# Kernel tuning notes

Hardware: AMD Instinct MI355X
Metric: run time of the kernel (lower is better)

The kernel has to match this reference:

```python
import jax, jax.numpy as jnp
import numpy as np

HID = 64   # hidden_dim
T = 256    # number of time points
B = 2048   # batch of initial conditions
DT = 0.05  # time step (t grid spacing)


def _xavier(k, shape, gain=0.5):
    fan_out, fan_in = shape
    std = gain * np.sqrt(2.0 / (fan_in + fan_out))
    return jax.random.normal(k, shape, dtype=jnp.float32) * std


def setup_inputs() -> dict:
    key = jax.random.key(0)
    ks = jax.random.split(key, 4)
    return {
        "t": jnp.arange(T, dtype=jnp.float32) * DT,
        "x0": jax.random.normal(ks[0], (B, 2), dtype=jnp.float32),
        "W1": _xavier(ks[1], (HID, 2)),
        "b1": jnp.zeros((HID,), jnp.float32),
        "W2": _xavier(ks[2], (HID, HID)),
        "b2": jnp.zeros((HID,), jnp.float32),
        "W3": _xavier(ks[3], (1, HID)),
        "b3": jnp.zeros((1,), jnp.float32),
    }


def reference(t, x0, W1, b1, W2, b2, W3, b3):
    """RK4 rollout of Hamiltonian dynamics. Returns trajectory [T, B, 2]."""

    def dynamics(x):
        h1 = jnp.tanh(x @ W1.T + b1)          # [B, H]
        h2 = jnp.tanh(h1 @ W2.T + b2)         # [B, H]
        # Analytic dH/dx via reverse chain (equivalent to autograd.grad):
        g2 = (1.0 - h2 * h2) * W3[0]          # [B, H]
        g1 = (1.0 - h1 * h1) * (g2 @ W2)      # [B, H]
        dHdx = g1 @ W1                        # [B, 2]  -> (dH/dq, dH/dp)
        # Hamilton's equations: dq/dt = dH/dp, dp/dt = -dH/dq
        return jnp.stack([dHdx[..., 1], -dHdx[..., 0]], axis=-1)

    dt = t[1] - t[0]

    def step(x, _):
        k1 = dynamics(x)
        k2 = dynamics(x + 0.5 * dt * k1)
        k3 = dynamics(x + 0.5 * dt * k2)
        k4 = dynamics(x + dt * k3)
        x_new = x + (dt / 6.0) * (k1 + 2.0 * k2 + 2.0 * k3 + k4)
        return x_new, x_new

    _, ys = jax.lax.scan(step, x0, None, length=t.shape[0] - 1)
    return jnp.concatenate([x0[None], ys], axis=0)  # [T, B, 2]
```

## Files before the change

kernel.cpp:

```cpp
#include <hip/hip_runtime.h>

#define HID    64
#define TSTEPS 256
#define BATCH  2048

typedef float v2f __attribute__((ext_vector_type(2)));

__device__ __forceinline__ float fast_tanh(float x) {
    float e = __builtin_amdgcn_exp2f(x * 2.8853900817779268f);
    float r = __builtin_amdgcn_rcpf(e + 1.0f);
    return fmaf(-2.0f, r, 1.0f);
}

template <int M>
__device__ __forceinline__ float swz(float v) {
    return __int_as_float(__builtin_amdgcn_ds_swizzle(
        __float_as_int(v), (M << 10) | 0x1F));
}
template <int M>
__device__ __forceinline__ v2f swz2(v2f v) {
    v2f r; r.x = swz<M>(v.x); r.y = swz<M>(v.y); return r;
}

template <int CTRL>
__device__ __forceinline__ float dppf(float x) {
    int xi = __float_as_int(x);
    return __int_as_float(__builtin_amdgcn_update_dpp(xi, xi, CTRL, 0xF, 0xF, false));
}
template <int CTRL>
__device__ __forceinline__ v2f dpp2(v2f v) {
    v2f r; r.x = dppf<CTRL>(v.x); r.y = dppf<CTRL>(v.y); return r;
}

__device__ __forceinline__ float bperm(int addr, float v) {
    return __int_as_float(__builtin_amdgcn_ds_bpermute(addr, __float_as_int(v)));
}

__global__ __launch_bounds__(256, 2) void hnn_rk4_kernel(
        const float* __restrict__ tarr,
        const float* __restrict__ x0,
        const float* __restrict__ W1,
        const float* __restrict__ b1,
        const float* __restrict__ W2,
        const float* __restrict__ b2,
        const float* __restrict__ W3,
        float* __restrict__ out)
{
    const int lane = threadIdx.x & 63;
    const int wid  = threadIdx.x >> 6;
    const int b    = blockIdx.x * 4 + wid;

    const int r0 = (lane >> 3) << 3;
    const int c0 = (lane & 7) << 3;

    const float dt  = tarr[1] - tarr[0];
    const float hdt = 0.5f * dt;
    const float sdt = dt * (1.0f / 6.0f);

    v2f   w1v = *(const v2f*)(W1 + 2 * lane);
    float b1i = b1[lane];
    float b2i = b2[lane];
    float w3i = W3[lane];

    int ba[8];
#pragma unroll
    for (int t = 0; t < 8; ++t) ba[t] = (c0 + t) * 4;
    int a32 = (lane ^ 32) * 4;

    v2f wfT[32], wbT[32];
#pragma unroll
    for (int t = 0; t < 8; ++t) {
#pragma unroll
        for (int m = 0; m < 4; ++m) {
            v2f f;
            f.x = W2[(r0 + 2 * m)     * HID + c0 + t];
            f.y = W2[(r0 + 2 * m + 1) * HID + c0 + t];
            wfT[t * 4 + m] = f;
            wbT[t * 4 + m] = *(const v2f*)(W2 + (c0 + t) * HID + r0 + 2 * m);
        }
    }

#pragma unroll
    for (int k = 0; k < 32; ++k) {
        asm volatile("" : "+v"(wfT[k]), "+v"(wbT[k]));
    }
#pragma unroll
    for (int t = 0; t < 8; ++t) asm volatile("" : "+v"(ba[t]));
    asm volatile("" : "+v"(w1v), "+v"(b1i), "+v"(b2i), "+v"(w3i), "+v"(a32));

    const bool s1b = lane & 1, s2b = lane & 2, s4b = lane & 4;

    auto reduce_pairs = [&](v2f P0, v2f P1, v2f P2, v2f P3) -> float {
        v2f kA0 = s2b ? P1 : P0,  sA0 = s2b ? P0 : P1;
        v2f kA1 = s2b ? P3 : P2,  sA1 = s2b ? P2 : P3;
        v2f g0 = kA0 + dpp2<0x4E>(sA0);
        v2f g1 = kA1 + dpp2<0x4E>(sA1);
        v2f kB = s4b ? g1 : g0,   sB = s4b ? g0 : g1;
        v2f h  = kB + swz2<4>(sB);
        v2f vf = h + dpp2<0xB1>(h);
        return s1b ? vf.y : vf.x;
    };

    float q = x0[2 * b + 0];
    float p = x0[2 * b + 1];

    if (lane == 0) {
        out[2 * b + 0] = q;
        out[2 * b + 1] = p;
    }

    auto dynamics = [&](float xq, float xp, float& kq, float& kp) {
        const float h1 = fast_tanh(fmaf(w1v.x, xq, fmaf(w1v.y, xp, b1i)));

        float hb[8];
#pragma unroll
        for (int t = 0; t < 8; ++t) hb[t] = bperm(ba[t], h1);

        v2f P0 = {0.f, 0.f}, P1 = {0.f, 0.f}, P2 = {0.f, 0.f}, P3 = {0.f, 0.f};
#pragma unroll
        for (int t = 0; t < 8; ++t) {
            v2f hh; hh.x = hb[t]; hh.y = hb[t];
            P0 = __builtin_elementwise_fma(wfT[t * 4 + 0], hh, P0);
            P1 = __builtin_elementwise_fma(wfT[t * 4 + 1], hh, P1);
            P2 = __builtin_elementwise_fma(wfT[t * 4 + 2], hh, P2);
            P3 = __builtin_elementwise_fma(wfT[t * 4 + 3], hh, P3);
        }
        const float pre2 = reduce_pairs(P0, P1, P2, P3) + b2i;
        const float h2   = fast_tanh(pre2);
        const float g2   = w3i * fmaf(-h2, h2, 1.0f);

        float gb[8];
#pragma unroll
        for (int t = 0; t < 8; ++t) gb[t] = bperm(ba[t], g2);

        v2f Q0 = {0.f, 0.f}, Q1 = {0.f, 0.f}, Q2 = {0.f, 0.f}, Q3 = {0.f, 0.f};
#pragma unroll
        for (int t = 0; t < 8; ++t) {
            v2f gg; gg.x = gb[t]; gg.y = gb[t];
            Q0 = __builtin_elementwise_fma(wbT[t * 4 + 0], gg, Q0);
            Q1 = __builtin_elementwise_fma(wbT[t * 4 + 1], gg, Q1);
            Q2 = __builtin_elementwise_fma(wbT[t * 4 + 2], gg, Q2);
            Q3 = __builtin_elementwise_fma(wbT[t * 4 + 3], gg, Q3);
        }
        const float u  = reduce_pairs(Q0, Q1, Q2, Q3);
        const float g1 = u * fmaf(-h1, h1, 1.0f);

        v2f gv; gv.x = g1; gv.y = g1;
        v2f sv = w1v * gv;
        sv = sv + dpp2<0xB1>(sv);
        sv = sv + dpp2<0x4E>(sv);
        sv = sv + swz2<4>(sv);
        sv = sv + swz2<8>(sv);
        sv = sv + swz2<16>(sv);
        v2f sw; sw.x = bperm(a32, sv.x); sw.y = bperm(a32, sv.y);
        sv = sv + sw;
        kq = sv.y;
        kp = -sv.x;
    };

#pragma unroll 1
    for (int s = 0; s < TSTEPS - 1; ++s) {
        float kq1, kp1, kq2, kp2, kq3, kp3, kq4, kp4;
        dynamics(q, p, kq1, kp1);
        dynamics(fmaf(hdt, kq1, q), fmaf(hdt, kp1, p), kq2, kp2);
        dynamics(fmaf(hdt, kq2, q), fmaf(hdt, kp2, p), kq3, kp3);
        dynamics(fmaf(dt,  kq3, q), fmaf(dt,  kp3, p), kq4, kp4);
        q = fmaf(sdt, kq1 + 2.f * kq2 + 2.f * kq3 + kq4, q);
        p = fmaf(sdt, kp1 + 2.f * kp2 + 2.f * kp3 + kp4, p);
        if (lane == 0) {
            out[(s + 1) * (BATCH * 2) + 2 * b + 0] = q;
            out[(s + 1) * (BATCH * 2) + 2 * b + 1] = p;
        }
    }
}

extern "C" void kernel_launch(void* const* d_in, const int* in_sizes, int n_in,
                              void* d_out, int out_size, void* d_ws, size_t ws_size,
                              hipStream_t stream) {
    const float* t  = (const float*)d_in[0];
    const float* x0 = (const float*)d_in[1];
    const float* W1 = (const float*)d_in[2];
    const float* b1 = (const float*)d_in[3];
    const float* W2 = (const float*)d_in[4];
    const float* b2 = (const float*)d_in[5];
    const float* W3 = (const float*)d_in[6];

    hnn_rk4_kernel<<<dim3(BATCH / 4), dim3(256), 0, stream>>>(
        t, x0, W1, b1, W2, b2, W3, (float*)d_out);
}
```

Baseline: 830.1 us.

## Reuse forward W2 tile for backward matvec, dropping the transposed W2 copy

The backward product g2 @ W2 now reuses the same per-lane W2 tile as the forward pass. Each lane broadcasts g2 along the row index instead of the column index, and the partial sums are reduced across row groups with DPP, swizzle and bpermute, followed by a bit-reversed permute to restore lane order. This removes the 32 extra v2f registers that held the transposed W2 copy, freeing registers and possibly allowing higher occupancy. In exchange the backward reduction uses more cross-lane operations, and one swizzle in the final reduction becomes a DPP row operation.

Result: slower. 869.4 us (+4.7%).

```diff
diff --git a/kernel.cpp b/kernel.cpp
--- a/kernel.cpp
+++ b/kernel.cpp
@@ -50,8 +50,8 @@
     const int wid  = threadIdx.x >> 6;
     const int b    = blockIdx.x * 4 + wid;
 
-    const int r0 = (lane >> 3) << 3;
-    const int c0 = (lane & 7) << 3;
+    const int rr = lane >> 3,  cc = lane & 7;
+    const int r0 = rr << 3,    c0 = cc << 3;
 
     const float dt  = tarr[1] - tarr[0];
     const float hdt = 0.5f * dt;
@@ -62,12 +62,17 @@
     float b2i = b2[lane];
     float w3i = W3[lane];
 
-    int ba[8];
-#pragma unroll
-    for (int t = 0; t < 8; ++t) ba[t] = (c0 + t) * 4;
+    int ba[8], br[8];
+#pragma unroll
+    for (int t = 0; t < 8; ++t) {
+        ba[t] = (c0 + t) * 4;
+        br[t] = (r0 + t) * 4;
+    }
     int a32 = (lane ^ 32) * 4;
-
-    v2f wfT[32], wbT[32];
+    const int rv = ((cc & 1) << 2) | (cc & 2) | ((cc >> 2) & 1);
+    int atr = (8 * rv + rr) * 4;
+
+    v2f wfT[32];
 #pragma unroll
     for (int t = 0; t < 8; ++t) {
 #pragma unroll
@@ -76,19 +81,11 @@
             f.x = W2[(r0 + 2 * m)     * HID + c0 + t];
             f.y = W2[(r0 + 2 * m + 1) * HID + c0 + t];
             wfT[t * 4 + m] = f;
-            wbT[t * 4 + m] = *(const v2f*)(W2 + (c0 + t) * HID + r0 + 2 * m);
-        }
-    }
-
-#pragma unroll
-    for (int k = 0; k < 32; ++k) {
-        asm volatile("" : "+v"(wfT[k]), "+v"(wbT[k]));
-    }
-#pragma unroll
-    for (int t = 0; t < 8; ++t) asm volatile("" : "+v"(ba[t]));
-    asm volatile("" : "+v"(w1v), "+v"(b1i), "+v"(b2i), "+v"(w3i), "+v"(a32));
-
-    const bool s1b = lane & 1, s2b = lane & 2, s4b = lane & 4;
+        }
+    }
+
+    const bool s1b = lane & 1,  s2b = lane & 2,  s4b = lane & 4;
+    const bool rb0 = lane & 8,  rb1 = lane & 16, rb2 = lane & 32;
 
     auto reduce_pairs = [&](v2f P0, v2f P1, v2f P2, v2f P3) -> float {
         v2f kA0 = s2b ? P1 : P0,  sA0 = s2b ? P0 : P1;
@@ -127,22 +124,43 @@
         }
         const float pre2 = reduce_pairs(P0, P1, P2, P3) + b2i;
         const float h2   = fast_tanh(pre2);
-        const float g2   = w3i * fmaf(-h2, h2, 1.0f);
+        const float g2v  = w3i * fmaf(-h2, h2, 1.0f);
 
         float gb[8];
 #pragma unroll
-        for (int t = 0; t < 8; ++t) gb[t] = bperm(ba[t], g2);
-
-        v2f Q0 = {0.f, 0.f}, Q1 = {0.f, 0.f}, Q2 = {0.f, 0.f}, Q3 = {0.f, 0.f};
+        for (int t = 0; t < 8; ++t) gb[t] = bperm(br[t], g2v);
+        v2f gp[4];
+#pragma unroll
+        for (int m = 0; m < 4; ++m) { gp[m].x = gb[2 * m]; gp[m].y = gb[2 * m + 1]; }
+
+        float uP[8];
 #pragma unroll
         for (int t = 0; t < 8; ++t) {
-            v2f gg; gg.x = gb[t]; gg.y = gb[t];
-            Q0 = __builtin_elementwise_fma(wbT[t * 4 + 0], gg, Q0);
-            Q1 = __builtin_elementwise_fma(wbT[t * 4 + 1], gg, Q1);
-            Q2 = __builtin_elementwise_fma(wbT[t * 4 + 2], gg, Q2);
-            Q3 = __builtin_elementwise_fma(wbT[t * 4 + 3], gg, Q3);
-        }
-        const float u  = reduce_pairs(Q0, Q1, Q2, Q3);
+            v2f acc = gp[0] * wfT[t * 4 + 0];
+            acc = __builtin_elementwise_fma(gp[1], wfT[t * 4 + 1], acc);
+            acc = __builtin_elementwise_fma(gp[2], wfT[t * 4 + 2], acc);
+            acc = __builtin_elementwise_fma(gp[3], wfT[t * 4 + 3], acc);
+            uP[t] = acc.x + acc.y;
+        }
+
+        float v4[4];
+#pragma unroll
+        for (int t = 0; t < 4; ++t) {
+            float keep = rb0 ? uP[t + 4] : uP[t];
+            float send = rb0 ? uP[t]     : uP[t + 4];
+            v4[t] = keep + dppf<0x128>(send);
+        }
+        float w2v[2];
+#pragma unroll
+        for (int k = 0; k < 2; ++k) {
+            float keep = rb1 ? v4[k + 2] : v4[k];
+            float send = rb1 ? v4[k]     : v4[k + 2];
+            w2v[k] = keep + swz<16>(send);
+        }
+        float keep3 = rb2 ? w2v[1] : w2v[0];
+        float send3 = rb2 ? w2v[0] : w2v[1];
+        float upre  = keep3 + bperm(a32, send3);
+        const float u  = bperm(atr, upre);
         const float g1 = u * fmaf(-h1, h1, 1.0f);
 
         v2f gv; gv.x = g1; gv.y = g1;
@@ -150,7 +168,7 @@
         sv = sv + dpp2<0xB1>(sv);
         sv = sv + dpp2<0x4E>(sv);
         sv = sv + swz2<4>(sv);
-        sv = sv + swz2<8>(sv);
+        sv = sv + dpp2<0x128>(sv);
         sv = sv + swz2<16>(sv);
         v2f sw; sw.x = bperm(a32, sv.x); sw.y = bperm(a32, sv.y);
         sv = sv + sw;
@@ -160,6 +178,12 @@
 
 #pragma unroll 1
     for (int s = 0; s < TSTEPS - 1; ++s) {
+#pragma unroll
+        for (int k = 0; k < 32; ++k) asm volatile("" : "+v"(wfT[k]));
+#pragma unroll
+        for (int t = 0; t < 8; ++t) asm volatile("" : "+v"(ba[t]), "+v"(br[t]));
+        asm volatile("" : "+v"(a32), "+v"(atr));
+
         float kq1, kp1, kq2, kp2, kq3, kp3, kq4, kp4;
         dynamics(q, p, kq1, kp1);
         dynamics(fmaf(hdt, kq1, q), fmaf(hdt, kp1, p), kq2, kp2);
```

## Permute hidden-unit layout to shorten cross-lane reductions and use DPP row-broadcast sums

Applied to the files above, without the earlier changes.

Reassigns hidden units to lanes with a bit-reversed permutation and stores W2 slices pre-XORed, so the partial-sum reductions after each 64x64 matvec need fewer, cheaper DPP/swizzle steps without lane-dependent selects. The final gradient reduction becomes a DPP row_shr/row_bcast scan followed by readlane, and inline v_pk_fma_f32 asm forces packed FMAs. It also drops the register-pinning asm barriers and changes launch bounds to 1 wave-group per CU minimum. This adds an extra bpermute to transpose the backward result and relies on the hand-written reduction being correct.

Measured after the change: 790.2 us. 1.05x faster.

```diff
diff --git a/kernel.cpp b/kernel.cpp
--- a/kernel.cpp
+++ b/kernel.cpp
@@ -17,26 +17,38 @@
     return __int_as_float(__builtin_amdgcn_ds_swizzle(
         __float_as_int(v), (M << 10) | 0x1F));
 }
-template <int M>
-__device__ __forceinline__ v2f swz2(v2f v) {
-    v2f r; r.x = swz<M>(v.x); r.y = swz<M>(v.y); return r;
-}
 
 template <int CTRL>
-__device__ __forceinline__ float dppf(float x) {
+__device__ __forceinline__ float dppx(float x) {
     int xi = __float_as_int(x);
     return __int_as_float(__builtin_amdgcn_update_dpp(xi, xi, CTRL, 0xF, 0xF, false));
-}
-template <int CTRL>
-__device__ __forceinline__ v2f dpp2(v2f v) {
-    v2f r; r.x = dppf<CTRL>(v.x); r.y = dppf<CTRL>(v.y); return r;
 }
 
 __device__ __forceinline__ float bperm(int addr, float v) {
     return __int_as_float(__builtin_amdgcn_ds_bpermute(addr, __float_as_int(v)));
 }
 
-__global__ __launch_bounds__(256, 2) void hnn_rk4_kernel(
+__device__ __forceinline__ void pkfma(v2f& acc, v2f w, v2f hv) {
+    asm("v_pk_fma_f32 %0, %1, %2, %0" : "+v"(acc) : "v"(w), "v"(hv));
+}
+
+__device__ __forceinline__ float wave_sum(float v) {
+    v += dppx<0x121>(v);
+    v += dppx<0x122>(v);
+    v += dppx<0x124>(v);
+    v += dppx<0x128>(v);
+    v += __int_as_float(__builtin_amdgcn_update_dpp(
+            0, __float_as_int(v), 0x142, 0xA, 0xF, false));
+    v += __int_as_float(__builtin_amdgcn_update_dpp(
+            0, __float_as_int(v), 0x143, 0xC, 0xF, false));
+    return __int_as_float(__builtin_amdgcn_readlane(__float_as_int(v), 63));
+}
+
+__device__ __forceinline__ int rev3(int x) {
+    return ((x & 1) << 2) | (x & 2) | ((x >> 2) & 1);
+}
+
+__global__ __launch_bounds__(256, 1) void hnn_rk4_kernel(
         const float* __restrict__ tarr,
         const float* __restrict__ x0,
         const float* __restrict__ W1,
@@ -50,56 +62,44 @@
     const int wid  = threadIdx.x >> 6;
     const int b    = blockIdx.x * 4 + wid;
 
-    const int r0 = (lane >> 3) << 3;
-    const int c0 = (lane & 7) << 3;
+    const int rr = lane >> 3, cc = lane & 7;
+    const int pc = rev3(cc),  pr = rev3(rr);
+    const int uo = 8 * rr + pc;
 
     const float dt  = tarr[1] - tarr[0];
     const float hdt = 0.5f * dt;
     const float sdt = dt * (1.0f / 6.0f);
 
-    v2f   w1v = *(const v2f*)(W1 + 2 * lane);
-    float b1i = b1[lane];
-    float b2i = b2[lane];
-    float w3i = W3[lane];
+    const float w1a = W1[2 * uo + 0];
+    const float w1b = W1[2 * uo + 1];
+    const float b1i = b1[uo];
+    const float b2i = b2[uo];
+    const float w3i = W3[uo];
 
-    int ba[8];
+    int ba[8], br[8];
 #pragma unroll
-    for (int t = 0; t < 8; ++t) ba[t] = (c0 + t) * 4;
+    for (int t = 0; t < 8; ++t) {
+        ba[t] = (8 * cc + rev3(t)) * 4;
+        br[t] = (8 * rr + rev3(t)) * 4;
+    }
     int a32 = (lane ^ 32) * 4;
+    int atr = (8 * cc + rr) * 4;
 
-    v2f wfT[32], wbT[32];
+    v2f wsF[8][4], wsB[8][4];
 #pragma unroll
     for (int t = 0; t < 8; ++t) {
 #pragma unroll
         for (int m = 0; m < 4; ++m) {
             v2f f;
-            f.x = W2[(r0 + 2 * m)     * HID + c0 + t];
-            f.y = W2[(r0 + 2 * m + 1) * HID + c0 + t];
-            wfT[t * 4 + m] = f;
-            wbT[t * 4 + m] = *(const v2f*)(W2 + (c0 + t) * HID + r0 + 2 * m);
+            f.x = W2[(8 * rr + ((2 * m)     ^ pc)) * HID + 8 * cc + t];
+            f.y = W2[(8 * rr + ((2 * m + 1) ^ pc)) * HID + 8 * cc + t];
+            wsF[t][m] = f;
+            v2f g;
+            g.x = W2[(8 * rr + t) * HID + 8 * cc + ((2 * m)     ^ pr)];
+            g.y = W2[(8 * rr + t) * HID + 8 * cc + ((2 * m + 1) ^ pr)];
+            wsB[t][m] = g;
         }
     }
-
-#pragma unroll
-    for (int k = 0; k < 32; ++k) {
-        asm volatile("" : "+v"(wfT[k]), "+v"(wbT[k]));
-    }
-#pragma unroll
-    for (int t = 0; t < 8; ++t) asm volatile("" : "+v"(ba[t]));
-    asm volatile("" : "+v"(w1v), "+v"(b1i), "+v"(b2i), "+v"(w3i), "+v"(a32));
-
-    const bool s1b = lane & 1, s2b = lane & 2, s4b = lane & 4;
-
-    auto reduce_pairs = [&](v2f P0, v2f P1, v2f P2, v2f P3) -> float {
-        v2f kA0 = s2b ? P1 : P0,  sA0 = s2b ? P0 : P1;
-        v2f kA1 = s2b ? P3 : P2,  sA1 = s2b ? P2 : P3;
-        v2f g0 = kA0 + dpp2<0x4E>(sA0);
-        v2f g1 = kA1 + dpp2<0x4E>(sA1);
-        v2f kB = s4b ? g1 : g0,   sB = s4b ? g0 : g1;
-        v2f h  = kB + swz2<4>(sB);
-        v2f vf = h + dpp2<0xB1>(h);
-        return s1b ? vf.y : vf.x;
-    };
 
     float q = x0[2 * b + 0];
     float p = x0[2 * b + 1];
@@ -110,7 +110,7 @@
     }
 
     auto dynamics = [&](float xq, float xp, float& kq, float& kp) {
-        const float h1 = fast_tanh(fmaf(w1v.x, xq, fmaf(w1v.y, xp, b1i)));
+        const float h1 = fast_tanh(fmaf(w1a, xq, fmaf(w1b, xp, b1i)));
 
         float hb[8];
 #pragma unroll
@@ -119,43 +119,42 @@
         v2f P0 = {0.f, 0.f}, P1 = {0.f, 0.f}, P2 = {0.f, 0.f}, P3 = {0.f, 0.f};
 #pragma unroll
         for (int t = 0; t < 8; ++t) {
-            v2f hh; hh.x = hb[t]; hh.y = hb[t];
-            P0 = __builtin_elementwise_fma(wfT[t * 4 + 0], hh, P0);
-            P1 = __builtin_elementwise_fma(wfT[t * 4 + 1], hh, P1);
-            P2 = __builtin_elementwise_fma(wfT[t * 4 + 2], hh, P2);
-            P3 = __builtin_elementwise_fma(wfT[t * 4 + 3], hh, P3);
+            v2f hv; hv.x = hb[t]; hv.y = hb[t];
+            pkfma(P0, wsF[t][0], hv);
+            pkfma(P1, wsF[t][1], hv);
+            pkfma(P2, wsF[t][2], hv);
+            pkfma(P3, wsF[t][3], hv);
         }
-        const float pre2 = reduce_pairs(P0, P1, P2, P3) + b2i;
-        const float h2   = fast_tanh(pre2);
-        const float g2   = w3i * fmaf(-h2, h2, 1.0f);
+        P0.x += dppx<0xB1>(P2.x);  P0.y += dppx<0xB1>(P2.y);
+        P1.x += dppx<0xB1>(P3.x);  P1.y += dppx<0xB1>(P3.y);
+        P0.x += dppx<0x4E>(P1.x);  P0.y += dppx<0x4E>(P1.y);
+        const float pre2 = P0.x + swz<4>(P0.y) + b2i;
+
+        const float h2 = fast_tanh(pre2);
+        const float g2 = w3i * fmaf(-h2, h2, 1.0f);
 
         float gb[8];
 #pragma unroll
-        for (int t = 0; t < 8; ++t) gb[t] = bperm(ba[t], g2);
+        for (int o = 0; o < 8; ++o) gb[o] = bperm(br[o], g2);
 
         v2f Q0 = {0.f, 0.f}, Q1 = {0.f, 0.f}, Q2 = {0.f, 0.f}, Q3 = {0.f, 0.f};
 #pragma unroll
-        for (int t = 0; t < 8; ++t) {
-            v2f gg; gg.x = gb[t]; gg.y = gb[t];
-            Q0 = __builtin_elementwise_fma(wbT[t * 4 + 0], gg, Q0);
-            Q1 = __builtin_elementwise_fma(wbT[t * 4 + 1], gg, Q1);
-            Q2 = __builtin_elementwise_fma(wbT[t * 4 + 2], gg, Q2);
-            Q3 = __builtin_elementwise_fma(wbT[t * 4 + 3], gg, Q3);
+        for (int o = 0; o < 8; ++o) {
+            v2f gv; gv.x = gb[o]; gv.y = gb[o];
+            pkfma(Q0, wsB[o][0], gv);
+            pkfma(Q1, wsB[o][1], gv);
+            pkfma(Q2, wsB[o][2], gv);
+            pkfma(Q3, wsB[o][3], gv);
         }
-        const float u  = reduce_pairs(Q0, Q1, Q2, Q3);
-        const float g1 = u * fmaf(-h1, h1, 1.0f);
+        Q0.x += dppx<0x128>(Q2.x);  Q0.y += dppx<0x128>(Q2.y);
+        Q1.x += dppx<0x128>(Q3.x);  Q1.y += dppx<0x128>(Q3.y);
+        Q0.x += swz<16>(Q1.x);      Q0.y += swz<16>(Q1.y);
+        const float upre = Q0.x + bperm(a32, Q0.y);
+        const float u    = bperm(atr, upre);
+        const float g1   = u * fmaf(-h1, h1, 1.0f);
 
-        v2f gv; gv.x = g1; gv.y = g1;
-        v2f sv = w1v * gv;
-        sv = sv + dpp2<0xB1>(sv);
-        sv = sv + dpp2<0x4E>(sv);
-        sv = sv + swz2<4>(sv);
-        sv = sv + swz2<8>(sv);
-        sv = sv + swz2<16>(sv);
-        v2f sw; sw.x = bperm(a32, sv.x); sw.y = bperm(a32, sv.y);
-        sv = sv + sw;
-        kq = sv.y;
-        kp = -sv.x;
+        kq =  wave_sum(g1 * w1b);
+        kp = -wave_sum(g1 * w1a);
     };
 
 #pragma unroll 1
@@ -165,8 +164,8 @@
         dynamics(fmaf(hdt, kq1, q), fmaf(hdt, kp1, p), kq2, kp2);
         dynamics(fmaf(hdt, kq2, q), fmaf(hdt, kp2, p), kq3, kp3);
         dynamics(fmaf(dt,  kq3, q), fmaf(dt,  kp3, p), kq4, kp4);
-        q = fmaf(sdt, kq1 + 2.f * kq2 + 2.f * kq3 + kq4, q);
-        p = fmaf(sdt, kp1 + 2.f * kp2 + 2.f * kp3 + kp4, p);
+        q = fmaf(sdt, (kq1 + kq4) + 2.0f * (kq2 + kq3), q);
+        p = fmaf(sdt, (kp1 + kp4) + 2.0f * (kp2 + kp3), p);
         if (lane == 0) {
             out[(s + 1) * (BATCH * 2) + 2 * b + 0] = q;
             out[(s + 1) * (BATCH * 2) + 2 * b + 1] = p;
```
